# Kernel tuning notes

Hardware: AMD Instinct MI355X
Metric: run time of the kernel (lower is better)

Reference implementation:

```python
import jax, jax.numpy as jnp
import numpy as np

NEG_SLOPE = 0.2  # PyG GATConv default negative_slope


def setup_inputs() -> dict:
    key = jax.random.key(0)
    k1, k2, k3, k4, k5 = jax.random.split(key, 5)
    N, E, IN, H, C = 50000, 800000, 128, 4, 64
    x = jax.random.normal(k1, (N, IN), dtype=jnp.float32)
    edge_index = jax.random.randint(k2, (2, E), 0, N, dtype=jnp.int32)
    W = jax.random.normal(k3, (IN, H * C), dtype=jnp.float32) * (1.0 / np.sqrt(IN))
    att_src = jax.random.normal(k4, (H, C), dtype=jnp.float32) * 0.1
    att_dst = jax.random.normal(k5, (H, C), dtype=jnp.float32) * 0.1
    bias = jnp.zeros((C,), dtype=jnp.float32)
    return {"x": x, "edge_index": edge_index, "W": W,
            "att_src": att_src, "att_dst": att_dst, "bias": bias}


def reference(x, edge_index, W, att_src, att_dst, bias):
    N = x.shape[0]
    H, C = att_src.shape
    # add self loops (PyG GATConv default add_self_loops=True)
    loop = jnp.arange(N, dtype=edge_index.dtype)
    src = jnp.concatenate([edge_index[0], loop])  # message source j
    dst = jnp.concatenate([edge_index[1], loop])  # message target i
    # linear projection, per-head view [N, H, C]
    h = (x @ W).reshape(N, H, C)
    # per-node attention terms [N, H]
    a_src = jnp.einsum('nhc,hc->nh', h, att_src)
    a_dst = jnp.einsum('nhc,hc->nh', h, att_dst)
    # per-edge logits with leaky relu [Etot, H]
    e = jax.nn.leaky_relu(a_src[src] + a_dst[dst], NEG_SLOPE)
    # segment softmax over incoming edges of each destination node
    emax = jax.ops.segment_max(e, dst, num_segments=N)       # [N, H]
    ex = jnp.exp(e - emax[dst])                              # [Etot, H]
    denom = jax.ops.segment_sum(ex, dst, num_segments=N)     # [N, H]
    alpha = ex / denom[dst]                                  # [Etot, H]
    # weighted scatter-aggregate of source features
    msg = h[src] * alpha[:, :, None]                         # [Etot, H, C]
    out = jax.ops.segment_sum(msg, dst, num_segments=N)      # [N, H, C]
    # concat=False -> mean over heads, then bias, then module-level ELU
    out = out.mean(axis=1) + bias
    return jax.nn.elu(out)
```

## Files before the change

kernel.cpp:

```cpp
#include <hip/hip_runtime.h>

#define NEG_SLOPE 0.2f
static constexpr int IN_F = 128;
static constexpr int NHEAD = 4;
static constexpr int CH = 64;
static constexpr int HC = 256;
static constexpr int SC_EPB = 2000;
static constexpr int CB_CAP = 6144;
static constexpr int CPAD = 16;

static __host__ size_t align256(size_t v) { return (v + 255) & ~((size_t)255); }

__device__ inline ushort f2bf(float f) {
    unsigned u = __float_as_uint(f);
    unsigned r = u + 0x7FFFu + ((u >> 16) & 1u);
    return (ushort)(r >> 16);
}
__device__ inline float bf2f(ushort s) { return __uint_as_float(((unsigned)s) << 16); }

typedef short s16x8 __attribute__((ext_vector_type(8)));
typedef float f32x16 __attribute__((ext_vector_type(16)));

__global__ __launch_bounds__(256) void prep_kernel(
    const float* __restrict__ W, ushort* __restrict__ Wt,
    int* __restrict__ ccnt, int* __restrict__ cur0,
    int* __restrict__ rowptr, int N, int Etot)
{
    int f = blockIdx.x * 256 + threadIdx.x;
    int k = f >> 8;
    int n = f & 255;
    Wt[n * IN_F + k] = f2bf(W[(size_t)k * HC + n]);
    if (f < 256 * CPAD) { ccnt[f] = 0; cur0[f] = 0; }
    if (f == 0) rowptr[N] = Etot;
}

__global__ __launch_bounds__(256) void gemm_mfma_kernel(
    const float* __restrict__ x, const ushort* __restrict__ Wt,
    const float* __restrict__ att_src, const float* __restrict__ att_dst,
    ushort* __restrict__ hb, float* __restrict__ a_src, float* __restrict__ a_dst,
    const int* __restrict__ dst, int* __restrict__ coarse_cnt,
    int E, int epb, int NTB, int NB, int N)
{
    constexpr int LDK = 136;
    __shared__ ushort As[64 * LDK];
    __shared__ ushort Bs[128 * LDK];
    ushort* Hs = As;

    const int t = threadIdx.x;

    if (blockIdx.x >= NTB) {
        int* hist = (int*)As;
        hist[t] = 0;
        __syncthreads();
        int slice = (blockIdx.x - NTB) * 2 + blockIdx.y;
        int lo = slice * epb;
        int hi = min(E, lo + epb);
        for (int i = lo + t; i < hi; i += 256)
            atomicAdd(&hist[((unsigned)dst[i]) >> 8], 1);
        __syncthreads();
        if (t < NB && hist[t]) atomicAdd(&coarse_cnt[t * CPAD], hist[t]);
        return;
    }

    const int m0 = blockIdx.x * 64;
    const int n0 = blockIdx.y * 128;

    #pragma unroll
    for (int u = 0; u < 8; ++u) {
        int f = t + 256 * u;
        int r = f >> 5;
        int k4 = (f & 31) * 4;
        int row = m0 + r;
        float4 v = make_float4(0.f, 0.f, 0.f, 0.f);
        if (row < N) v = *(const float4*)(x + (size_t)row * IN_F + k4);
        ushort4 o;
        o.x = f2bf(v.x); o.y = f2bf(v.y); o.z = f2bf(v.z); o.w = f2bf(v.w);
        *(ushort4*)&As[r * LDK + k4] = o;
    }
    #pragma unroll
    for (int u = 0; u < 8; ++u) {
        int f = t + 256 * u;
        int n = f >> 4;
        int k8 = (f & 15) * 8;
        uint4 v = *(const uint4*)(Wt + (size_t)(n0 + n) * IN_F + k8);
        *(uint4*)&Bs[n * LDK + k8] = v;
    }
    __syncthreads();

    const int w = t >> 6;
    const int lane = t & 63;
    const int mrow = 32 * (w >> 1) + (lane & 31);
    const int nbase = 64 * (w & 1) + (lane & 31);
    const int kq = (lane >> 5) * 8;

    f32x16 acc0 = {}, acc1 = {};
    #pragma unroll
    for (int s = 0; s < 8; ++s) {
        s16x8 af = *(const s16x8*)&As[mrow * LDK + 16 * s + kq];
        s16x8 b0 = *(const s16x8*)&Bs[nbase * LDK + 16 * s + kq];
        s16x8 b1 = *(const s16x8*)&Bs[(nbase + 32) * LDK + 16 * s + kq];
        acc0 = __builtin_amdgcn_mfma_f32_32x32x16_bf16(af, b0, acc0, 0, 0, 0);
        acc1 = __builtin_amdgcn_mfma_f32_32x32x16_bf16(af, b1, acc1, 0, 0, 0);
    }
    __syncthreads();

    {
        int rbase = 4 * (lane >> 5) + 32 * (w >> 1);
        int c0 = 64 * (w & 1) + (lane & 31);
        #pragma unroll
        for (int r = 0; r < 16; ++r) {
            int rowL = rbase + (r & 3) + 8 * (r >> 2);
            Hs[rowL * LDK + c0]      = f2bf(acc0[r]);
            Hs[rowL * LDK + c0 + 32] = f2bf(acc1[r]);
        }
    }
    __syncthreads();

    {
        int r2 = t >> 2;
        int q = t & 3;
        int row = m0 + r2;
        uint4 p0 = *(const uint4*)&Hs[r2 * LDK + 32 * q];
        uint4 p1 = *(const uint4*)&Hs[r2 * LDK + 32 * q + 8];
        uint4 p2 = *(const uint4*)&Hs[r2 * LDK + 32 * q + 16];
        uint4 p3 = *(const uint4*)&Hs[r2 * LDK + 32 * q + 24];
        if (row < N) {
            ushort* dsth = hb + (size_t)row * HC + n0 + 32 * q;
            *(uint4*)(dsth)      = p0;
            *(uint4*)(dsth + 8)  = p1;
            *(uint4*)(dsth + 16) = p2;
            *(uint4*)(dsth + 24) = p3;
        }
        int hq = 2 * blockIdx.y + (q >> 1);
        int cb = (q & 1) * 32;
        const float* asp = att_src + hq * CH + cb;
        const float* adp = att_dst + hq * CH + cb;
        unsigned uu[16] = { p0.x, p0.y, p0.z, p0.w, p1.x, p1.y, p1.z, p1.w,
                            p2.x, p2.y, p2.z, p2.w, p3.x, p3.y, p3.z, p3.w };
        float ps = 0.f, pd = 0.f;
        #pragma unroll
        for (int i = 0; i < 16; ++i) {
            float lo = bf2f((ushort)(uu[i] & 0xFFFFu));
            float hi = bf2f((ushort)(uu[i] >> 16));
            ps += lo * asp[2 * i] + hi * asp[2 * i + 1];
            pd += lo * adp[2 * i] + hi * adp[2 * i + 1];
        }
        ps += __shfl_xor(ps, 1, 64);
        pd += __shfl_xor(pd, 1, 64);
        if ((q & 1) == 0 && row < N) {
            a_src[(size_t)row * NHEAD + hq] = ps;
            a_dst[(size_t)row * NHEAD + hq] = pd;
        }
    }
}

__global__ __launch_bounds__(256) void bucket_scatter(
    const int* __restrict__ src, const int* __restrict__ dst,
    const int* __restrict__ ccnt, int* __restrict__ cur0,
    unsigned* __restrict__ ebuf, int E)
{
    __shared__ int eb[256];
    __shared__ int hist[256];
    __shared__ int lbase[256];
    __shared__ int gbase[256];
    __shared__ int cur[256];
    __shared__ unsigned sbuf[SC_EPB + 48];
    __shared__ unsigned char tb[SC_EPB + 48];
    int t = threadIdx.x;
    int cv = ccnt[t * CPAD];
    eb[t] = cv;
    __syncthreads();
    #pragma unroll
    for (int off = 1; off < 256; off <<= 1) {
        int a = eb[t];
        int b = (t >= off) ? eb[t - off] : 0;
        __syncthreads();
        eb[t] = a + b;
        __syncthreads();
    }
    int myebase = eb[t] - cv;
    __syncthreads();
    eb[t] = myebase;

    int lo = blockIdx.x * SC_EPB;
    int hi = min(E, lo + SC_EPB);
    int cnt = hi - lo;
    hist[t] = 0;
    __syncthreads();
    unsigned pk[8]; int bk[8];
    #pragma unroll
    for (int u = 0; u < 8; ++u) {
        int i = lo + t + 256 * u;
        bk[u] = -1;
        if (i < hi) {
            unsigned d = (unsigned)dst[i];
            bk[u] = (int)(d >> 8);
            pk[u] = (((unsigned)src[i]) << 8) | (d & 255u);
            atomicAdd(&hist[bk[u]], 1);
        }
    }
    __syncthreads();
    int v = hist[t];
    lbase[t] = v;
    __syncthreads();
    #pragma unroll
    for (int off = 1; off < 256; off <<= 1) {
        int a = lbase[t];
        int b = (t >= off) ? lbase[t - off] : 0;
        __syncthreads();
        lbase[t] = a + b;
        __syncthreads();
    }
    int excl = lbase[t] - v;
    if (v) gbase[t] = eb[t] + atomicAdd(&cur0[t * CPAD], v);
    __syncthreads();
    lbase[t] = excl;
    cur[t] = excl;
    __syncthreads();
    #pragma unroll
    for (int u = 0; u < 8; ++u) {
        if (bk[u] >= 0) {
            int p = atomicAdd(&cur[bk[u]], 1);
            sbuf[p] = pk[u];
            tb[p] = (unsigned char)bk[u];
        }
    }
    __syncthreads();
    for (int j = t; j < cnt; j += 256) {
        int b = tb[j];
        ebuf[gbase[b] + j - lbase[b]] = sbuf[j];
    }
}

__global__ __launch_bounds__(256) void csr_build(
    const unsigned* __restrict__ ebuf, const int* __restrict__ ccnt,
    int* __restrict__ rowptr, int* __restrict__ csr_src, int N)
{
    __shared__ int scn[256];
    __shared__ int hist[256];
    __shared__ int cur[256];
    __shared__ unsigned srt[CB_CAP];
    int b = blockIdx.x;
    int t = threadIdx.x;
    int cv = ccnt[t * CPAD];
    scn[t] = cv;
    __syncthreads();
    #pragma unroll
    for (int off = 1; off < 256; off <<= 1) {
        int a = scn[t];
        int bb = (t >= off) ? scn[t - off] : 0;
        __syncthreads();
        scn[t] = a + bb;
        __syncthreads();
    }
    int lo = (b == 0) ? 0 : scn[b - 1];
    int hi = scn[b];
    __syncthreads();

    int n0 = b << 8;
    int ncnt = min(256, N - n0);
    int cnt = hi - lo;
    int cb = lo + n0;
    hist[t] = 0;
    __syncthreads();
    for (int i = lo + t; i < hi; i += 256)
        atomicAdd(&hist[ebuf[i] & 255u], 1);
    __syncthreads();
    int v = hist[t];
    scn[t] = v;
    __syncthreads();
    #pragma unroll
    for (int off = 1; off < 256; off <<= 1) {
        int a = scn[t];
        int bb = (t >= off) ? scn[t - off] : 0;
        __syncthreads();
        scn[t] = a + bb;
        __syncthreads();
    }
    int excl = scn[t] - v;
    if (t < ncnt) {
        int segstart = cb + excl + t;
        rowptr[n0 + t] = segstart;
        csr_src[segstart] = n0 + t;
    }
    cur[t] = excl;
    __syncthreads();
    if (cnt <= CB_CAP) {
        for (int i = lo + t; i < hi; i += 256) {
            unsigned e = ebuf[i];
            int p = atomicAdd(&cur[e & 255u], 1);
            srt[p] = e;
        }
        __syncthreads();
        for (int j = t; j < cnt; j += 256) {
            unsigned e = srt[j];
            csr_src[cb + j + (int)(e & 255u) + 1] = (int)(e >> 8);
        }
    } else {
        for (int i = lo + t; i < hi; i += 256) {
            unsigned e = ebuf[i];
            int ln = (int)(e & 255u);
            int p = atomicAdd(&cur[ln], 1);
            csr_src[cb + p + ln + 1] = (int)(e >> 8);
        }
    }
}

__global__ __launch_bounds__(256) void aggregate_kernel(
    const ushort* __restrict__ hb, const float* __restrict__ a_src,
    const float* __restrict__ a_dst, const int* __restrict__ rowptr,
    const int* __restrict__ csr_src, const float* __restrict__ bias,
    float* __restrict__ out, int N)
{
    int node = (int)((blockIdx.x * (size_t)blockDim.x + threadIdx.x) >> 6);
    int l = threadIdx.x & 63;
    if (node >= N) return;
    int start = rowptr[node];
    int end = rowptr[node + 1];
    int hd = l >> 4;
    float adh = a_dst[(size_t)node * NHEAD + hd];

    float4 acc0 = make_float4(0.f, 0.f, 0.f, 0.f);
    float4 acc1 = make_float4(0.f, 0.f, 0.f, 0.f);
    float4 acc2 = make_float4(0.f, 0.f, 0.f, 0.f);
    float4 acc3 = make_float4(0.f, 0.f, 0.f, 0.f);
    float s0 = 0.f, s1 = 0.f, s2 = 0.f, s3 = 0.f;

    int k = start;
    for (; k + 4 <= end; k += 4) {
        int sj0 = csr_src[k];
        int sj1 = csr_src[k + 1];
        int sj2 = csr_src[k + 2];
        int sj3 = csr_src[k + 3];
        float a0 = a_src[(size_t)sj0 * NHEAD + hd];
        float a1 = a_src[(size_t)sj1 * NHEAD + hd];
        float a2 = a_src[(size_t)sj2 * NHEAD + hd];
        float a3 = a_src[(size_t)sj3 * NHEAD + hd];
        ushort4 h0 = *(const ushort4*)(hb + ((size_t)sj0 << 8) + 4 * l);
        ushort4 h1 = *(const ushort4*)(hb + ((size_t)sj1 << 8) + 4 * l);
        ushort4 h2 = *(const ushort4*)(hb + ((size_t)sj2 << 8) + 4 * l);
        ushort4 h3 = *(const ushort4*)(hb + ((size_t)sj3 << 8) + 4 * l);
        float e0 = a0 + adh; e0 = fmaxf(e0, NEG_SLOPE * e0); float w0 = __expf(e0);
        float e1 = a1 + adh; e1 = fmaxf(e1, NEG_SLOPE * e1); float w1 = __expf(e1);
        float e2 = a2 + adh; e2 = fmaxf(e2, NEG_SLOPE * e2); float w2 = __expf(e2);
        float e3 = a3 + adh; e3 = fmaxf(e3, NEG_SLOPE * e3); float w3 = __expf(e3);
        s0 += w0; s1 += w1; s2 += w2; s3 += w3;
        acc0.x += w0 * bf2f(h0.x); acc0.y += w0 * bf2f(h0.y);
        acc0.z += w0 * bf2f(h0.z); acc0.w += w0 * bf2f(h0.w);
        acc1.x += w1 * bf2f(h1.x); acc1.y += w1 * bf2f(h1.y);
        acc1.z += w1 * bf2f(h1.z); acc1.w += w1 * bf2f(h1.w);
        acc2.x += w2 * bf2f(h2.x); acc2.y += w2 * bf2f(h2.y);
        acc2.z += w2 * bf2f(h2.z); acc2.w += w2 * bf2f(h2.w);
        acc3.x += w3 * bf2f(h3.x); acc3.y += w3 * bf2f(h3.y);
        acc3.z += w3 * bf2f(h3.z); acc3.w += w3 * bf2f(h3.w);
    }
    for (; k < end; ++k) {
        int sj0 = csr_src[k];
        float a0 = a_src[(size_t)sj0 * NHEAD + hd];
        ushort4 h0 = *(const ushort4*)(hb + ((size_t)sj0 << 8) + 4 * l);
        float e0 = a0 + adh; e0 = fmaxf(e0, NEG_SLOPE * e0);
        float w0 = __expf(e0);
        s0 += w0;
        acc0.x += w0 * bf2f(h0.x); acc0.y += w0 * bf2f(h0.y);
        acc0.z += w0 * bf2f(h0.z); acc0.w += w0 * bf2f(h0.w);
    }

    float inv = 1.0f / (s0 + s1 + s2 + s3);
    float4 acc;
    acc.x = (acc0.x + acc1.x + acc2.x + acc3.x) * inv;
    acc.y = (acc0.y + acc1.y + acc2.y + acc3.y) * inv;
    acc.z = (acc0.z + acc1.z + acc2.z + acc3.z) * inv;
    acc.w = (acc0.w + acc1.w + acc2.w + acc3.w) * inv;

    #pragma unroll
    for (int off = 16; off < 64; off <<= 1) {
        acc.x += __shfl_xor(acc.x, off, 64);
        acc.y += __shfl_xor(acc.y, off, 64);
        acc.z += __shfl_xor(acc.z, off, 64);
        acc.w += __shfl_xor(acc.w, off, 64);
    }
    if (l < 16) {
        float4 b4 = *(const float4*)(bias + 4 * l);
        float4 o;
        o.x = acc.x * 0.25f + b4.x;
        o.y = acc.y * 0.25f + b4.y;
        o.z = acc.z * 0.25f + b4.z;
        o.w = acc.w * 0.25f + b4.w;
        o.x = (o.x > 0.f) ? o.x : (__expf(o.x) - 1.f);
        o.y = (o.y > 0.f) ? o.y : (__expf(o.y) - 1.f);
        o.z = (o.z > 0.f) ? o.z : (__expf(o.z) - 1.f);
        o.w = (o.w > 0.f) ? o.w : (__expf(o.w) - 1.f);
        *(float4*)(out + (size_t)node * CH + 4 * l) = o;
    }
}

extern "C" void kernel_launch(void* const* d_in, const int* in_sizes, int n_in,
                              void* d_out, int out_size, void* d_ws, size_t ws_size,
                              hipStream_t stream)
{
    const float* x         = (const float*)d_in[0];
    const int*   edge_idx  = (const int*)d_in[1];
    const float* W         = (const float*)d_in[2];
    const float* att_src   = (const float*)d_in[3];
    const float* att_dst   = (const float*)d_in[4];
    const float* bias      = (const float*)d_in[5];
    float* out = (float*)d_out;

    const int N = in_sizes[0] / IN_F;
    const int E = in_sizes[1] / 2;
    const int Etot = E + N;
    const int NB = (N + 255) >> 8;
    const int* srcp = edge_idx;
    const int* dstp = edge_idx + E;

    char* ws = (char*)d_ws;
    size_t off = 0;
    ushort*  hb     = (ushort*)(ws + off);   off += align256((size_t)N * HC * sizeof(ushort));
    ushort*  Wt     = (ushort*)(ws + off);   off += align256((size_t)HC * IN_F * sizeof(ushort));
    float*   a_src  = (float*)(ws + off);    off += align256((size_t)N * NHEAD * sizeof(float));
    float*   a_dst  = (float*)(ws + off);    off += align256((size_t)N * NHEAD * sizeof(float));
    int*     ccnt   = (int*)(ws + off);      off += align256(256 * CPAD * sizeof(int));
    int*     cur0   = (int*)(ws + off);      off += align256(256 * CPAD * sizeof(int));
    unsigned* ebuf  = (unsigned*)(ws + off); off += align256((size_t)E * sizeof(unsigned));
    int*     rowptr = (int*)(ws + off);      off += align256(((size_t)N + 1) * sizeof(int));
    int*     csrs   = (int*)(ws + off);      off += align256((size_t)Etot * sizeof(int));
    (void)ws_size; (void)n_in; (void)out_size;

    const int NTB = (N + 63) / 64;
    const int PBC = 208;
    const int epbc = (E + 2 * PBC - 1) / (2 * PBC);
    const int PBS = (E + SC_EPB - 1) / SC_EPB;

    prep_kernel<<<IN_F * HC / 256, 256, 0, stream>>>(W, Wt, ccnt, cur0, rowptr, N, Etot);
    dim3 gg(NTB + PBC, 2);
    gemm_mfma_kernel<<<gg, 256, 0, stream>>>(x, Wt, att_src, att_dst, hb,
                                             a_src, a_dst, dstp, ccnt,
                                             E, epbc, NTB, NB, N);
    bucket_scatter<<<PBS, 256, 0, stream>>>(srcp, dstp, ccnt, cur0, ebuf, E);
    csr_build<<<NB, 256, 0, stream>>>(ebuf, ccnt, rowptr, csrs, N);
    aggregate_kernel<<<((size_t)N * 64 + 255) / 256, 256, 0, stream>>>(
        hb, a_src, a_dst, rowptr, csrs, bias, out, N);
}
```

Baseline: 201.0 us.

## Reschedule stages: fuse W prep with edge counting, co-launch GEMM with CSR build

Moves the coarse destination histogram out of the GEMM launch and into the W-transpose prep kernel, and zeroes the counters with a memset instead. The CSR build blocks are merged into the GEMM launch as extra blocks, so the dense projection overlaps the sort-based CSR construction. The intent is fewer dependent launches and better overlap of compute-bound and memory-bound stages. The trade-off is a larger shared-memory footprint for the CSR blocks, which now use the GEMM-sized allocation, and possible imbalance between the two block types.

```diff
diff --git a/kernel.cpp b/kernel.cpp
--- a/kernel.cpp
+++ b/kernel.cpp
@@ -8,6 +8,8 @@
 static constexpr int SC_EPB = 2000;
 static constexpr int CB_CAP = 6144;
 static constexpr int CPAD = 16;
+static constexpr int PBC = 416;
+static constexpr int PREPB = 128;
 
 static __host__ size_t align256(size_t v) { return (v + 255) & ~((size_t)255); }
 
@@ -21,137 +23,30 @@
 typedef short s16x8 __attribute__((ext_vector_type(8)));
 typedef float f32x16 __attribute__((ext_vector_type(16)));
 
-__global__ __launch_bounds__(256) void prep_kernel(
+__global__ __launch_bounds__(256) void prep_count_kernel(
     const float* __restrict__ W, ushort* __restrict__ Wt,
-    int* __restrict__ ccnt, int* __restrict__ cur0,
-    int* __restrict__ rowptr, int N, int Etot)
+    const int* __restrict__ dst, int* __restrict__ ccnt,
+    int* __restrict__ rowptr, int N, int Etot, int E, int epb, int NB)
 {
-    int f = blockIdx.x * 256 + threadIdx.x;
-    int k = f >> 8;
-    int n = f & 255;
-    Wt[n * IN_F + k] = f2bf(W[(size_t)k * HC + n]);
-    if (f < 256 * CPAD) { ccnt[f] = 0; cur0[f] = 0; }
-    if (f == 0) rowptr[N] = Etot;
-}
-
-__global__ __launch_bounds__(256) void gemm_mfma_kernel(
-    const float* __restrict__ x, const ushort* __restrict__ Wt,
-    const float* __restrict__ att_src, const float* __restrict__ att_dst,
-    ushort* __restrict__ hb, float* __restrict__ a_src, float* __restrict__ a_dst,
-    const int* __restrict__ dst, int* __restrict__ coarse_cnt,
-    int E, int epb, int NTB, int NB, int N)
-{
-    constexpr int LDK = 136;
-    __shared__ ushort As[64 * LDK];
-    __shared__ ushort Bs[128 * LDK];
-    ushort* Hs = As;
-
-    const int t = threadIdx.x;
-
-    if (blockIdx.x >= NTB) {
-        int* hist = (int*)As;
-        hist[t] = 0;
-        __syncthreads();
-        int slice = (blockIdx.x - NTB) * 2 + blockIdx.y;
-        int lo = slice * epb;
-        int hi = min(E, lo + epb);
-        for (int i = lo + t; i < hi; i += 256)
-            atomicAdd(&hist[((unsigned)dst[i]) >> 8], 1);
-        __syncthreads();
-        if (t < NB && hist[t]) atomicAdd(&coarse_cnt[t * CPAD], hist[t]);
+    __shared__ int hist[256];
+    int t = threadIdx.x;
+    if (blockIdx.x < PREPB) {
+        int f = blockIdx.x * 256 + t;
+        int k = f >> 8;
+        int n = f & 255;
+        Wt[n * IN_F + k] = f2bf(W[(size_t)k * HC + n]);
+        if (f == 0) rowptr[N] = Etot;
         return;
     }
-
-    const int m0 = blockIdx.x * 64;
-    const int n0 = blockIdx.y * 128;
-
-    #pragma unroll
-    for (int u = 0; u < 8; ++u) {
-        int f = t + 256 * u;
-        int r = f >> 5;
-        int k4 = (f & 31) * 4;
-        int row = m0 + r;
-        float4 v = make_float4(0.f, 0.f, 0.f, 0.f);
-        if (row < N) v = *(const float4*)(x + (size_t)row * IN_F + k4);
-        ushort4 o;
-        o.x = f2bf(v.x); o.y = f2bf(v.y); o.z = f2bf(v.z); o.w = f2bf(v.w);
-        *(ushort4*)&As[r * LDK + k4] = o;
-    }
-    #pragma unroll
-    for (int u = 0; u < 8; ++u) {
-        int f = t + 256 * u;
-        int n = f >> 4;
-        int k8 = (f & 15) * 8;
-        uint4 v = *(const uint4*)(Wt + (size_t)(n0 + n) * IN_F + k8);
-        *(uint4*)&Bs[n * LDK + k8] = v;
-    }
-    __syncthreads();
-
-    const int w = t >> 6;
-    const int lane = t & 63;
-    const int mrow = 32 * (w >> 1) + (lane & 31);
-    const int nbase = 64 * (w & 1) + (lane & 31);
-    const int kq = (lane >> 5) * 8;
-
-    f32x16 acc0 = {}, acc1 = {};
-    #pragma unroll
-    for (int s = 0; s < 8; ++s) {
-        s16x8 af = *(const s16x8*)&As[mrow * LDK + 16 * s + kq];
-        s16x8 b0 = *(const s16x8*)&Bs[nbase * LDK + 16 * s + kq];
-        s16x8 b1 = *(const s16x8*)&Bs[(nbase + 32) * LDK + 16 * s + kq];
-        acc0 = __builtin_amdgcn_mfma_f32_32x32x16_bf16(af, b0, acc0, 0, 0, 0);
-        acc1 = __builtin_amdgcn_mfma_f32_32x32x16_bf16(af, b1, acc1, 0, 0, 0);
-    }
-    __syncthreads();
-
-    {
-        int rbase = 4 * (lane >> 5) + 32 * (w >> 1);
-        int c0 = 64 * (w & 1) + (lane & 31);
-        #pragma unroll
-        for (int r = 0; r < 16; ++r) {
-            int rowL = rbase + (r & 3) + 8 * (r >> 2);
-            Hs[rowL * LDK + c0]      = f2bf(acc0[r]);
-            Hs[rowL * LDK + c0 + 32] = f2bf(acc1[r]);
-        }
-    }
-    __syncthreads();
-
-    {
-        int r2 = t >> 2;
-        int q = t & 3;
-        int row = m0 + r2;
-        uint4 p0 = *(const uint4*)&Hs[r2 * LDK + 32 * q];
-        uint4 p1 = *(const uint4*)&Hs[r2 * LDK + 32 * q + 8];
-        uint4 p2 = *(const uint4*)&Hs[r2 * LDK + 32 * q + 16];
-        uint4 p3 = *(const uint4*)&Hs[r2 * LDK + 32 * q + 24];
-        if (row < N) {
-            ushort* dsth = hb + (size_t)row * HC + n0 + 32 * q;
-            *(uint4*)(dsth)      = p0;
-            *(uint4*)(dsth + 8)  = p1;
-            *(uint4*)(dsth + 16) = p2;
-            *(uint4*)(dsth + 24) = p3;
-        }
-        int hq = 2 * blockIdx.y + (q >> 1);
-        int cb = (q & 1) * 32;
-        const float* asp = att_src + hq * CH + cb;
-        const float* adp = att_dst + hq * CH + cb;
-        unsigned uu[16] = { p0.x, p0.y, p0.z, p0.w, p1.x, p1.y, p1.z, p1.w,
-                            p2.x, p2.y, p2.z, p2.w, p3.x, p3.y, p3.z, p3.w };
-        float ps = 0.f, pd = 0.f;
-        #pragma unroll
-        for (int i = 0; i < 16; ++i) {
-            float lo = bf2f((ushort)(uu[i] & 0xFFFFu));
-            float hi = bf2f((ushort)(uu[i] >> 16));
-            ps += lo * asp[2 * i] + hi * asp[2 * i + 1];
-            pd += lo * adp[2 * i] + hi * adp[2 * i + 1];
-        }
-        ps += __shfl_xor(ps, 1, 64);
-        pd += __shfl_xor(pd, 1, 64);
-        if ((q & 1) == 0 && row < N) {
-            a_src[(size_t)row * NHEAD + hq] = ps;
-            a_dst[(size_t)row * NHEAD + hq] = pd;
-        }
-    }
+    hist[t] = 0;
+    __syncthreads();
+    int slice = blockIdx.x - PREPB;
+    int lo = slice * epb;
+    int hi = min(E, lo + epb);
+    for (int i = lo + t; i < hi; i += 256)
+        atomicAdd(&hist[((unsigned)dst[i]) >> 8], 1);
+    __syncthreads();
+    if (t < NB && hist[t]) atomicAdd(&ccnt[t * CPAD], hist[t]);
 }
 
 __global__ __launch_bounds__(256) void bucket_scatter(
@@ -232,76 +127,182 @@
     }
 }
 
-__global__ __launch_bounds__(256) void csr_build(
+__global__ __launch_bounds__(256) void gemm_csr_kernel(
+    const float* __restrict__ x, const ushort* __restrict__ Wt,
+    const float* __restrict__ att_src, const float* __restrict__ att_dst,
+    ushort* __restrict__ hb, float* __restrict__ a_src, float* __restrict__ a_dst,
     const unsigned* __restrict__ ebuf, const int* __restrict__ ccnt,
-    int* __restrict__ rowptr, int* __restrict__ csr_src, int N)
+    int* __restrict__ rowptr, int* __restrict__ csr_src,
+    int NTB, int NB, int N)
 {
-    __shared__ int scn[256];
-    __shared__ int hist[256];
-    __shared__ int cur[256];
-    __shared__ unsigned srt[CB_CAP];
-    int b = blockIdx.x;
-    int t = threadIdx.x;
-    int cv = ccnt[t * CPAD];
-    scn[t] = cv;
-    __syncthreads();
-    #pragma unroll
-    for (int off = 1; off < 256; off <<= 1) {
-        int a = scn[t];
-        int bb = (t >= off) ? scn[t - off] : 0;
-        __syncthreads();
-        scn[t] = a + bb;
-        __syncthreads();
-    }
-    int lo = (b == 0) ? 0 : scn[b - 1];
-    int hi = scn[b];
-    __syncthreads();
-
-    int n0 = b << 8;
-    int ncnt = min(256, N - n0);
-    int cnt = hi - lo;
-    int cb = lo + n0;
-    hist[t] = 0;
-    __syncthreads();
-    for (int i = lo + t; i < hi; i += 256)
-        atomicAdd(&hist[ebuf[i] & 255u], 1);
-    __syncthreads();
-    int v = hist[t];
-    scn[t] = v;
-    __syncthreads();
-    #pragma unroll
-    for (int off = 1; off < 256; off <<= 1) {
-        int a = scn[t];
-        int bb = (t >= off) ? scn[t - off] : 0;
-        __syncthreads();
-        scn[t] = a + bb;
-        __syncthreads();
-    }
-    int excl = scn[t] - v;
-    if (t < ncnt) {
-        int segstart = cb + excl + t;
-        rowptr[n0 + t] = segstart;
-        csr_src[segstart] = n0 + t;
-    }
-    cur[t] = excl;
-    __syncthreads();
-    if (cnt <= CB_CAP) {
-        for (int i = lo + t; i < hi; i += 256) {
-            unsigned e = ebuf[i];
-            int p = atomicAdd(&cur[e & 255u], 1);
-            srt[p] = e;
-        }
-        __syncthreads();
-        for (int j = t; j < cnt; j += 256) {
-            unsigned e = srt[j];
-            csr_src[cb + j + (int)(e & 255u) + 1] = (int)(e >> 8);
-        }
-    } else {
-        for (int i = lo + t; i < hi; i += 256) {
-            unsigned e = ebuf[i];
-            int ln = (int)(e & 255u);
-            int p = atomicAdd(&cur[ln], 1);
-            csr_src[cb + p + ln + 1] = (int)(e >> 8);
+    constexpr int LDK = 136;
+    __shared__ __align__(16) char smem[64 * LDK * 2 + 128 * LDK * 2];
+    const int t = threadIdx.x;
+
+    if (blockIdx.x >= NTB) {
+        int b = (blockIdx.x - NTB) * 2 + blockIdx.y;
+        if (b >= NB) return;
+        int* scn = (int*)smem;
+        int* hist = (int*)(smem + 1024);
+        int* cur = (int*)(smem + 2048);
+        unsigned* srt = (unsigned*)(smem + 3072);
+        int cv = ccnt[t * CPAD];
+        scn[t] = cv;
+        __syncthreads();
+        #pragma unroll
+        for (int off = 1; off < 256; off <<= 1) {
+            int a = scn[t];
+            int bb = (t >= off) ? scn[t - off] : 0;
+            __syncthreads();
+            scn[t] = a + bb;
+            __syncthreads();
+        }
+        int lo = (b == 0) ? 0 : scn[b - 1];
+        int hi = scn[b];
+        __syncthreads();
+
+        int n0 = b << 8;
+        int ncnt = min(256, N - n0);
+        int cnt = hi - lo;
+        int cb = lo + n0;
+        hist[t] = 0;
+        __syncthreads();
+        for (int i = lo + t; i < hi; i += 256)
+            atomicAdd(&hist[ebuf[i] & 255u], 1);
+        __syncthreads();
+        int v = hist[t];
+        scn[t] = v;
+        __syncthreads();
+        #pragma unroll
+        for (int off = 1; off < 256; off <<= 1) {
+            int a = scn[t];
+            int bb = (t >= off) ? scn[t - off] : 0;
+            __syncthreads();
+            scn[t] = a + bb;
+            __syncthreads();
+        }
+        int excl = scn[t] - v;
+        if (t < ncnt) {
+            int segstart = cb + excl + t;
+            rowptr[n0 + t] = segstart;
+            csr_src[segstart] = n0 + t;
+        }
+        cur[t] = excl;
+        __syncthreads();
+        if (cnt <= CB_CAP) {
+            for (int i = lo + t; i < hi; i += 256) {
+                unsigned e = ebuf[i];
+                int p = atomicAdd(&cur[e & 255u], 1);
+                srt[p] = e;
+            }
+            __syncthreads();
+            for (int j = t; j < cnt; j += 256) {
+                unsigned e = srt[j];
+                csr_src[cb + j + (int)(e & 255u) + 1] = (int)(e >> 8);
+            }
+        } else {
+            for (int i = lo + t; i < hi; i += 256) {
+                unsigned e = ebuf[i];
+                int ln = (int)(e & 255u);
+                int p = atomicAdd(&cur[ln], 1);
+                csr_src[cb + p + ln + 1] = (int)(e >> 8);
+            }
+        }
+        return;
+    }
+
+    ushort* As = (ushort*)smem;
+    ushort* Bs = (ushort*)(smem + 64 * LDK * 2);
+    ushort* Hs = As;
+
+    const int m0 = blockIdx.x * 64;
+    const int n0 = blockIdx.y * 128;
+
+    #pragma unroll
+    for (int u = 0; u < 8; ++u) {
+        int f = t + 256 * u;
+        int r = f >> 5;
+        int k4 = (f & 31) * 4;
+        int row = m0 + r;
+        float4 v = make_float4(0.f, 0.f, 0.f, 0.f);
+        if (row < N) v = *(const float4*)(x + (size_t)row * IN_F + k4);
+        ushort4 o;
+        o.x = f2bf(v.x); o.y = f2bf(v.y); o.z = f2bf(v.z); o.w = f2bf(v.w);
+        *(ushort4*)&As[r * LDK + k4] = o;
+    }
+    #pragma unroll
+    for (int u = 0; u < 8; ++u) {
+        int f = t + 256 * u;
+        int n = f >> 4;
+        int k8 = (f & 15) * 8;
+        uint4 v = *(const uint4*)(Wt + (size_t)(n0 + n) * IN_F + k8);
+        *(uint4*)&Bs[n * LDK + k8] = v;
+    }
+    __syncthreads();
+
+    const int w = t >> 6;
+    const int lane = t & 63;
+    const int mrow = 32 * (w >> 1) + (lane & 31);
+    const int nbase = 64 * (w & 1) + (lane & 31);
+    const int kq = (lane >> 5) * 8;
+
+    f32x16 acc0 = {}, acc1 = {};
+    #pragma unroll
+    for (int s = 0; s < 8; ++s) {
+        s16x8 af = *(const s16x8*)&As[mrow * LDK + 16 * s + kq];
+        s16x8 b0 = *(const s16x8*)&Bs[nbase * LDK + 16 * s + kq];
+        s16x8 b1 = *(const s16x8*)&Bs[(nbase + 32) * LDK + 16 * s + kq];
+        acc0 = __builtin_amdgcn_mfma_f32_32x32x16_bf16(af, b0, acc0, 0, 0, 0);
+        acc1 = __builtin_amdgcn_mfma_f32_32x32x16_bf16(af, b1, acc1, 0, 0, 0);
+    }
+    __syncthreads();
+
+    {
+        int rbase = 4 * (lane >> 5) + 32 * (w >> 1);
+        int c0 = 64 * (w & 1) + (lane & 31);
+        #pragma unroll
+        for (int r = 0; r < 16; ++r) {
+            int rowL = rbase + (r & 3) + 8 * (r >> 2);
+            Hs[rowL * LDK + c0]      = f2bf(acc0[r]);
+            Hs[rowL * LDK + c0 + 32] = f2bf(acc1[r]);
+        }
+    }
+    __syncthreads();
+
+    {
+        int r2 = t >> 2;
+        int q = t & 3;
+        int row = m0 + r2;
+        uint4 p0 = *(const uint4*)&Hs[r2 * LDK + 32 * q];
+        uint4 p1 = *(const uint4*)&Hs[r2 * LDK + 32 * q + 8];
+        uint4 p2 = *(const uint4*)&Hs[r2 * LDK + 32 * q + 16];
+        uint4 p3 = *(const uint4*)&Hs[r2 * LDK + 32 * q + 24];
+        if (row < N) {
+            ushort* dsth = hb + (size_t)row * HC + n0 + 32 * q;
+            *(uint4*)(dsth)      = p0;
+            *(uint4*)(dsth + 8)  = p1;
+            *(uint4*)(dsth + 16) = p2;
+            *(uint4*)(dsth + 24) = p3;
+        }
+        int hq = 2 * blockIdx.y + (q >> 1);
+        int cb = (q & 1) * 32;
+        const float* asp = att_src + hq * CH + cb;
+        const float* adp = att_dst + hq * CH + cb;
+        unsigned uu[16] = { p0.x, p0.y, p0.z, p0.w, p1.x, p1.y, p1.z, p1.w,
+                            p2.x, p2.y, p2.z, p2.w, p3.x, p3.y, p3.z, p3.w };
+        float ps = 0.f, pd = 0.f;
+        #pragma unroll
+        for (int i = 0; i < 16; ++i) {
+            float lo = bf2f((ushort)(uu[i] & 0xFFFFu));
+            float hi = bf2f((ushort)(uu[i] >> 16));
+            ps += lo * asp[2 * i] + hi * asp[2 * i + 1];
+            pd += lo * adp[2 * i] + hi * adp[2 * i + 1];
+        }
+        ps += __shfl_xor(ps, 1, 64);
+        pd += __shfl_xor(pd, 1, 64);
+        if ((q & 1) == 0 && row < N) {
+            a_src[(size_t)row * NHEAD + hq] = ps;
+            a_dst[(size_t)row * NHEAD + hq] = pd;
         }
     }
 }
@@ -427,17 +428,18 @@
     (void)ws_size; (void)n_in; (void)out_size;
 
     const int NTB = (N + 63) / 64;
-    const int PBC = 208;
-    const int epbc = (E + 2 * PBC - 1) / (2 * PBC);
+    const int epbc = (E + PBC - 1) / PBC;
     const int PBS = (E + SC_EPB - 1) / SC_EPB;
-
-    prep_kernel<<<IN_F * HC / 256, 256, 0, stream>>>(W, Wt, ccnt, cur0, rowptr, N, Etot);
-    dim3 gg(NTB + PBC, 2);
-    gemm_mfma_kernel<<<gg, 256, 0, stream>>>(x, Wt, att_src, att_dst, hb,
-                                             a_src, a_dst, dstp, ccnt,
-                                             E, epbc, NTB, NB, N);
+    const int NBH = (NB + 1) / 2;
+
+    hipMemsetAsync(ccnt, 0, 2 * 256 * CPAD * sizeof(int), stream);
+    prep_count_kernel<<<PREPB + PBC, 256, 0, stream>>>(
+        W, Wt, dstp, ccnt, rowptr, N, Etot, E, epbc, NB);
     bucket_scatter<<<PBS, 256, 0, stream>>>(srcp, dstp, ccnt, cur0, ebuf, E);
-    csr_build<<<NB, 256, 0, stream>>>(ebuf, ccnt, rowptr, csrs, N);
+    dim3 gg(NTB + NBH, 2);
+    gemm_csr_kernel<<<gg, 256, 0, stream>>>(x, Wt, att_src, att_dst, hb,
+                                            a_src, a_dst, ebuf, ccnt,
+                                            rowptr, csrs, NTB, NB, N);
     aggregate_kernel<<<((size_t)N * 64 + 255) / 256, 256, 0, stream>>>(
         hb, a_src, a_dst, rowptr, csrs, bias, out, N);
 }
```

New measurement: 206.9 us. 1.03x slower.
